# Performance work log

Hardware: AMD Instinct MI355X
Metric: run time of the kernel (lower is better)

Reference implementation:

```python
import jax, jax.numpy as jnp
import numpy as np

N, M, FIN, K, OUT, E = 8, 49152, 64, 6, 64, 393216


def setup_inputs() -> dict:
    key = jax.random.key(0)
    k1, k2, k3, k4, k5, k6 = jax.random.split(key, 6)
    x = jax.random.normal(k1, (N, M, FIN), jnp.float32)
    rows = jax.random.randint(k2, (E,), 0, M, jnp.int32)
    cols = jax.random.randint(k3, (E,), 0, M, jnp.int32)
    vals = jax.random.normal(k4, (E,), jnp.float32) * 0.1  # scaled-Laplacian values
    stdv = 1.0 / np.sqrt(OUT)
    weight = jax.random.uniform(k5, (FIN * K, OUT), jnp.float32, -stdv, stdv)
    bias = jax.random.uniform(k6, (OUT,), jnp.float32, -stdv, stdv)
    return {"x": x, "rows": rows, "cols": cols, "vals": vals,
            "weight": weight, "bias": bias}


def reference(x, rows, cols, vals, weight, bias):
    # x: [N, M, Fin]; L sparse [M, M] in COO (rows, cols, vals)
    n, m, fin = x.shape
    # x0: [M, Fin*N] as in torch permute(1,2,0).view(M, Fin*N)
    x0 = jnp.transpose(x, (1, 2, 0)).reshape(m, fin * n)

    def spmm(X):  # L @ X via gather + segment-sum scatter
        return jax.ops.segment_sum(vals[:, None] * X[cols], rows, num_segments=m)

    xs = [x0]
    if K > 1:
        x1 = spmm(x0)
        xs.append(x1)
        for _ in range(2, K):
            x2 = 2.0 * spmm(x1) - x0
            xs.append(x2)
            x0, x1 = x1, x2

    # stack -> [K, M, Fin, N]; torch then permutes to [N, M, Fin, K] and
    # flattens to (N*M, Fin*K) with Fin outer, K inner: weight row idx = f*K + k
    T = jnp.stack(xs, 0).reshape(K, m, fin, n)
    Wr = weight.reshape(fin, K, OUT)
    out = jnp.einsum('kmfn,fko->nmo', T, Wr) + bias  # [N, M, OUT]
    return jax.nn.elu(out)
```

## Files before the change

kernel.cpp:

```cpp
#include <hip/hip_runtime.h>
#include <hip/hip_bf16.h>
#include <math.h>

#define N_    8
#define M_    49152
#define FIN_  64
#define K_    6
#define OUT_  64
#define E_    393216
#define ROW_  512

typedef __attribute__((ext_vector_type(8))) short bf16x8;
typedef __attribute__((ext_vector_type(4))) float f32x4;

static __device__ __forceinline__ unsigned short f2bf(float f) {
    unsigned u = __float_as_uint(f);
    u += 0x7fff + ((u >> 16) & 1);
    return (unsigned short)(u >> 16);
}
static __device__ __forceinline__ float bfl(unsigned u) { return __uint_as_float(u << 16); }
static __device__ __forceinline__ float bfh(unsigned u) { return __uint_as_float(u & 0xffff0000u); }


__global__ void count_kernel(const int* __restrict__ rows, int* __restrict__ cnt) {
    int e = blockIdx.x * blockDim.x + threadIdx.x;
    if (e < E_) atomicAdd(&cnt[rows[e]], 1);
}

__global__ __launch_bounds__(1024) void scan_kernel(int* __restrict__ cntfill, int* __restrict__ rowptr) {
    __shared__ int wsum[16];
    __shared__ int carry;
    int t = threadIdx.x;
    int lane = t & 63, wid = t >> 6;
    if (t == 0) carry = 0;
    __syncthreads();
    for (int chunk = 0; chunk < M_; chunk += 1024) {
        int v = cntfill[chunk + t];
        int x = v;
        #pragma unroll
        for (int off = 1; off < 64; off <<= 1) {
            int y = __shfl_up(x, off, 64);
            if (lane >= off) x += y;
        }
        if (lane == 63) wsum[wid] = x;
        __syncthreads();
        if (t == 0) {
            int s = carry;
            #pragma unroll
            for (int i = 0; i < 16; ++i) { int c = wsum[i]; wsum[i] = s; s += c; }
            carry = s;
        }
        __syncthreads();
        int excl = wsum[wid] + x - v;
        rowptr[chunk + t]  = excl;
        cntfill[chunk + t] = excl;
        __syncthreads();
    }
    if (t == 0) rowptr[M_] = carry;
}

__global__ void fill_kernel(const int* __restrict__ rows, const int* __restrict__ cols,
                            const float* __restrict__ vals, int* __restrict__ fillpos,
                            int* __restrict__ ecol, float* __restrict__ evalv,
                            int* __restrict__ eidx) {
    int e = blockIdx.x * blockDim.x + threadIdx.x;
    if (e < E_) {
        int r = rows[e];
        int p = atomicAdd(&fillpos[r], 1);
        ecol[p]  = cols[e];
        evalv[p] = vals[e];
        eidx[p]  = e;
    }
}

__global__ void sort_kernel(const int* __restrict__ rowptr, int* __restrict__ ecol,
                            float* __restrict__ evalv, int* __restrict__ eidx) {
    int m = blockIdx.x * blockDim.x + threadIdx.x;
    if (m >= M_) return;
    int s = rowptr[m], e = rowptr[m + 1];
    for (int i = s + 1; i < e; ++i) {
        int ki = eidx[i]; int kc = ecol[i]; float kv = evalv[i];
        int j = i - 1;
        while (j >= s && eidx[j] > ki) {
            eidx[j + 1] = eidx[j]; ecol[j + 1] = ecol[j]; evalv[j + 1] = evalv[j];
            --j;
        }
        eidx[j + 1] = ki; ecol[j + 1] = kc; evalv[j + 1] = kv;
    }
}


__global__ void permute_bf16_kernel(const float* __restrict__ x, unsigned short* __restrict__ T0) {
    int idx = blockIdx.x * blockDim.x + threadIdx.x;
    int f4 = idx & 15, n = (idx >> 4) & 7, m = idx >> 7;
    float4 v = ((const float4*)x)[(size_t)(n * M_ + m) * 16 + f4];
    ushort4 o;
    o.x = f2bf(v.x); o.y = f2bf(v.y); o.z = f2bf(v.z); o.w = f2bf(v.w);
    *(ushort4*)(T0 + (size_t)m * ROW_ + n * 64 + f4 * 4) = o;
}

static __device__ __forceinline__ void fma_u4(float* acc, float v, uint4 u) {
    acc[0] += v * bfl(u.x); acc[1] += v * bfh(u.x);
    acc[2] += v * bfl(u.y); acc[3] += v * bfh(u.y);
    acc[4] += v * bfl(u.z); acc[5] += v * bfh(u.z);
    acc[6] += v * bfl(u.w); acc[7] += v * bfh(u.w);
}

__global__ __launch_bounds__(256) void spmm_bf16_kernel(
        const unsigned short* __restrict__ cur, const unsigned short* __restrict__ prev,
        unsigned short* __restrict__ nxt,
        const int* __restrict__ rowptr, const int* __restrict__ ecol,
        const float* __restrict__ evalv, float alpha, float beta) {
    int t = threadIdx.x;
    int w = t >> 6, l = t & 63;
    int m = blockIdx.x * 4 + w;
    int s = rowptr[m], e = rowptr[m + 1];
    float acc[8] = {0.f, 0.f, 0.f, 0.f, 0.f, 0.f, 0.f, 0.f};
    int i = s;
    for (; i + 3 < e; i += 4) {
        int c0 = ecol[i], c1 = ecol[i+1], c2 = ecol[i+2], c3 = ecol[i+3];
        float v0 = evalv[i], v1 = evalv[i+1], v2 = evalv[i+2], v3 = evalv[i+3];
        uint4 u0 = *(const uint4*)(cur + (size_t)c0 * ROW_ + l * 8);
        uint4 u1 = *(const uint4*)(cur + (size_t)c1 * ROW_ + l * 8);
        uint4 u2 = *(const uint4*)(cur + (size_t)c2 * ROW_ + l * 8);
        uint4 u3 = *(const uint4*)(cur + (size_t)c3 * ROW_ + l * 8);
        fma_u4(acc, v0, u0); fma_u4(acc, v1, u1);
        fma_u4(acc, v2, u2); fma_u4(acc, v3, u3);
    }
    if (i + 1 < e) {
        int c0 = ecol[i], c1 = ecol[i+1];
        float v0 = evalv[i], v1 = evalv[i+1];
        uint4 u0 = *(const uint4*)(cur + (size_t)c0 * ROW_ + l * 8);
        uint4 u1 = *(const uint4*)(cur + (size_t)c1 * ROW_ + l * 8);
        fma_u4(acc, v0, u0); fma_u4(acc, v1, u1);
        i += 2;
    }
    if (i < e) {
        uint4 u0 = *(const uint4*)(cur + (size_t)ecol[i] * ROW_ + l * 8);
        fma_u4(acc, evalv[i], u0);
    }
    #pragma unroll
    for (int j = 0; j < 8; ++j) acc[j] *= alpha;
    if (beta != 0.f) {
        uint4 p = *(const uint4*)(prev + (size_t)m * ROW_ + l * 8);
        acc[0] += beta * bfl(p.x); acc[1] += beta * bfh(p.x);
        acc[2] += beta * bfl(p.y); acc[3] += beta * bfh(p.y);
        acc[4] += beta * bfl(p.z); acc[5] += beta * bfh(p.z);
        acc[6] += beta * bfl(p.w); acc[7] += beta * bfh(p.w);
    }
    uint4 o;
    o.x = (unsigned)f2bf(acc[0]) | ((unsigned)f2bf(acc[1]) << 16);
    o.y = (unsigned)f2bf(acc[2]) | ((unsigned)f2bf(acc[3]) << 16);
    o.z = (unsigned)f2bf(acc[4]) | ((unsigned)f2bf(acc[5]) << 16);
    o.w = (unsigned)f2bf(acc[6]) | ((unsigned)f2bf(acc[7]) << 16);
    *(uint4*)(nxt + (size_t)m * ROW_ + l * 8) = o;
}

__global__ void wprep_kernel(const float* __restrict__ W, unsigned short* __restrict__ Wfrag) {
    int idx = blockIdx.x * blockDim.x + threadIdx.x;
    int i = idx & 7, l = (idx >> 3) & 63, tile = (idx >> 9) & 3, kk = idx >> 11;
    int kcheb = kk >> 1;
    int f = (kk & 1) * 32 + (l >> 4) * 8 + i;
    int o = tile * 16 + (l & 15);
    Wfrag[idx] = f2bf(W[(f * K_ + kcheb) * OUT_ + o]);
}

static __device__ __forceinline__ void epilogue_tile(
        f32x4 acc, int tile, int rbase, int col,
        const float* __restrict__ bias, float* __restrict__ outn) {
    int c = tile * 16 + col;
    float b = bias[c];
    #pragma unroll
    for (int v = 0; v < 4; ++v) {
        float r = acc[v] + b;
        r = r > 0.f ? r : (__expf(r) - 1.f);
        outn[(size_t)(rbase + v) * OUT_ + c] = r;
    }
}

__global__ __launch_bounds__(256) void combine_kernel(
        const unsigned short* __restrict__ Tbase,
        const unsigned short* __restrict__ Wfrag,
        const float* __restrict__ bias, float* __restrict__ out) {
    __shared__ unsigned short wlds[24576];
    int t = threadIdx.x;
    {
        const uint4* src = (const uint4*)Wfrag;
        uint4* dst = (uint4*)wlds;
        #pragma unroll
        for (int i = 0; i < 12; ++i)
            dst[t + 256 * i] = src[t + 256 * i];
    }
    __syncthreads();

    int w = t >> 6, l = t & 63;
    int rowhalf = w & 1, nhalf = w >> 1;
    int m0 = blockIdx.x * 32 + rowhalf * 16;
    int arow = m0 + (l & 15);
    const size_t MROW = (size_t)M_ * ROW_;
    size_t abase0 = (size_t)arow * ROW_ + (l >> 4) * 8;
    int rbase = m0 + (l >> 4) * 4;
    int col = l & 15;

    #pragma unroll
    for (int ni = 0; ni < 4; ++ni) {
        int n = nhalf * 4 + ni;
        size_t abase = abase0 + n * 64;
        bf16x8 a[12];
        #pragma unroll
        for (int kk = 0; kk < 12; ++kk)
            a[kk] = *(const bf16x8*)(Tbase + (size_t)(kk >> 1) * MROW + abase + (kk & 1) * 32);

        f32x4 acc0 = {0.f, 0.f, 0.f, 0.f};
        f32x4 acc1 = {0.f, 0.f, 0.f, 0.f};
        f32x4 acc2 = {0.f, 0.f, 0.f, 0.f};
        f32x4 acc3 = {0.f, 0.f, 0.f, 0.f};
        #pragma unroll
        for (int kk = 0; kk < 12; ++kk) {
            const unsigned short* wp = wlds + ((size_t)(kk * 4) * 64 + l) * 8;
            bf16x8 b0 = *(const bf16x8*)(wp);
            bf16x8 b1 = *(const bf16x8*)(wp + 512);
            bf16x8 b2 = *(const bf16x8*)(wp + 1024);
            bf16x8 b3 = *(const bf16x8*)(wp + 1536);
            acc0 = __builtin_amdgcn_mfma_f32_16x16x32_bf16(a[kk], b0, acc0, 0, 0, 0);
            acc1 = __builtin_amdgcn_mfma_f32_16x16x32_bf16(a[kk], b1, acc1, 0, 0, 0);
            acc2 = __builtin_amdgcn_mfma_f32_16x16x32_bf16(a[kk], b2, acc2, 0, 0, 0);
            acc3 = __builtin_amdgcn_mfma_f32_16x16x32_bf16(a[kk], b3, acc3, 0, 0, 0);
        }

        float* outn = out + (size_t)n * ((size_t)M_ * OUT_);
        epilogue_tile(acc0, 0, rbase, col, bias, outn);
        epilogue_tile(acc1, 1, rbase, col, bias, outn);
        epilogue_tile(acc2, 2, rbase, col, bias, outn);
        epilogue_tile(acc3, 3, rbase, col, bias, outn);
    }
}


__global__ void permute_kernel(const float* __restrict__ x, float* __restrict__ A) {
    int idx = blockIdx.x * blockDim.x + threadIdx.x;
    int f4 = idx & 15;
    int n  = (idx >> 4) & 7;
    int m  = idx >> 7;
    float4 v = ((const float4*)x)[(size_t)(n * M_ + m) * 16 + f4];
    ((float4*)A)[idx] = v;
}

__global__ __launch_bounds__(512) void step_kernel(
        const float* __restrict__ cur, float* __restrict__ nxt,
        const float* __restrict__ weight, const float* __restrict__ bias,
        const int* __restrict__ rowptr, const int* __restrict__ ecol,
        const float* __restrict__ evalv, float* __restrict__ out,
        int k, float alpha, float beta, int flags) {
    __shared__ float lds_x[ROW_];
    int m = blockIdx.x;
    int t = threadIdx.x;
    lds_x[t] = cur[(size_t)m * ROW_ + t];
    if (flags & 4) {
        float acc = 0.f;
        int s = rowptr[m], e = rowptr[m + 1];
        for (int i = s; i < e; ++i)
            acc += evalv[i] * cur[(size_t)ecol[i] * ROW_ + t];
        float prevv = (beta != 0.f) ? nxt[(size_t)m * ROW_ + t] : 0.f;
        nxt[(size_t)m * ROW_ + t] = alpha * acc + beta * prevv;
    }
    __syncthreads();
    int n = t >> 6, o = t & 63;
    const float4* lx4 = (const float4*)(lds_x + n * FIN_);
    float acc = 0.f;
    #pragma unroll
    for (int f4 = 0; f4 < 16; ++f4) {
        float4 xq = lx4[f4];
        int fb = f4 * 4;
        acc += xq.x * weight[((fb + 0) * K_ + k) * OUT_ + o];
        acc += xq.y * weight[((fb + 1) * K_ + k) * OUT_ + o];
        acc += xq.z * weight[((fb + 2) * K_ + k) * OUT_ + o];
        acc += xq.w * weight[((fb + 3) * K_ + k) * OUT_ + o];
    }
    size_t oidx = (size_t)n * (M_ * OUT_) + (size_t)m * OUT_ + o;
    float res = (flags & 1) ? acc : (out[oidx] + acc);
    if (flags & 2) {
        res += bias[o];
        res = (res > 0.f) ? res : (expf(res) - 1.f);
    }
    out[oidx] = res;
}


extern "C" void kernel_launch(void* const* d_in, const int* in_sizes, int n_in,
                              void* d_out, int out_size, void* d_ws, size_t ws_size,
                              hipStream_t stream) {
    (void)in_sizes; (void)n_in; (void)out_size;
    const float* x      = (const float*)d_in[0];
    const int*   rows   = (const int*)d_in[1];
    const int*   cols   = (const int*)d_in[2];
    const float* vals   = (const float*)d_in[3];
    const float* weight = (const float*)d_in[4];
    const float* bias   = (const float*)d_in[5];
    float* out = (float*)d_out;

    char* ws = (char*)d_ws;
    size_t off = 0;
    auto alloc = [&](size_t bytes) -> void* {
        void* p = ws + off;
        off += (bytes + 255) & ~(size_t)255;
        return p;
    };

    const size_t tbytes = (size_t)M_ * ROW_ * 2;
    const size_t need_new = 6 * (tbytes + 256) + (M_ + 1) * 4 + M_ * 4
                          + 3 * ((size_t)E_ * 4 + 256) + 24576 * 2 + 4096;

    if (ws_size >= need_new) {
        unsigned short* T[6];
        for (int i = 0; i < 6; ++i) T[i] = (unsigned short*)alloc(tbytes);
        int*   rowptr  = (int*)alloc((size_t)(M_ + 1) * 4);
        int*   fillpos = (int*)alloc((size_t)M_ * 4);
        int*   ecol    = (int*)alloc((size_t)E_ * 4);
        float* evalv   = (float*)alloc((size_t)E_ * 4);
        int*   eidx    = (int*)alloc((size_t)E_ * 4);
        unsigned short* Wfrag = (unsigned short*)alloc(24576 * 2);

        permute_bf16_kernel<<<(M_ * N_ * 16) / 256, 256, 0, stream>>>(x, T[0]);
        hipMemsetAsync(fillpos, 0, (size_t)M_ * 4, stream);
        count_kernel<<<E_ / 256, 256, 0, stream>>>(rows, fillpos);
        scan_kernel<<<1, 1024, 0, stream>>>(fillpos, rowptr);
        fill_kernel<<<E_ / 256, 256, 0, stream>>>(rows, cols, vals, fillpos, ecol, evalv, eidx);
        sort_kernel<<<M_ / 256, 256, 0, stream>>>(rowptr, ecol, evalv, eidx);
        wprep_kernel<<<96, 256, 0, stream>>>(weight, Wfrag);

        spmm_bf16_kernel<<<M_ / 4, 256, 0, stream>>>(T[0], T[0], T[1], rowptr, ecol, evalv, 1.f, 0.f);
        spmm_bf16_kernel<<<M_ / 4, 256, 0, stream>>>(T[1], T[0], T[2], rowptr, ecol, evalv, 2.f, -1.f);
        spmm_bf16_kernel<<<M_ / 4, 256, 0, stream>>>(T[2], T[1], T[3], rowptr, ecol, evalv, 2.f, -1.f);
        spmm_bf16_kernel<<<M_ / 4, 256, 0, stream>>>(T[3], T[2], T[4], rowptr, ecol, evalv, 2.f, -1.f);
        spmm_bf16_kernel<<<M_ / 4, 256, 0, stream>>>(T[4], T[3], T[5], rowptr, ecol, evalv, 2.f, -1.f);

        combine_kernel<<<M_ / 32, 256, 0, stream>>>(T[0], Wfrag, bias, out);
    } else {
        float* A       = (float*)alloc((size_t)M_ * ROW_ * 4);
        float* B       = (float*)alloc((size_t)M_ * ROW_ * 4);
        int*   rowptr  = (int*)alloc((size_t)(M_ + 1) * 4);
        int*   fillpos = (int*)alloc((size_t)M_ * 4);
        int*   ecol    = (int*)alloc((size_t)E_ * 4);
        float* evalv   = (float*)alloc((size_t)E_ * 4);
        int*   eidx    = (int*)alloc((size_t)E_ * 4);

        permute_kernel<<<(M_ * N_ * 16) / 256, 256, 0, stream>>>(x, A);
        hipMemsetAsync(fillpos, 0, (size_t)M_ * 4, stream);
        count_kernel<<<E_ / 256, 256, 0, stream>>>(rows, fillpos);
        scan_kernel<<<1, 1024, 0, stream>>>(fillpos, rowptr);
        fill_kernel<<<E_ / 256, 256, 0, stream>>>(rows, cols, vals, fillpos, ecol, evalv, eidx);
        sort_kernel<<<M_ / 256, 256, 0, stream>>>(rowptr, ecol, evalv, eidx);

        step_kernel<<<M_, 512, 0, stream>>>(A, B, weight, bias, rowptr, ecol, evalv, out, 0, 1.f, 0.f, 1 | 4);
        step_kernel<<<M_, 512, 0, stream>>>(B, A, weight, bias, rowptr, ecol, evalv, out, 1, 2.f, -1.f, 4);
        step_kernel<<<M_, 512, 0, stream>>>(A, B, weight, bias, rowptr, ecol, evalv, out, 2, 2.f, -1.f, 4);
        step_kernel<<<M_, 512, 0, stream>>>(B, A, weight, bias, rowptr, ecol, evalv, out, 3, 2.f, -1.f, 4);
        step_kernel<<<M_, 512, 0, stream>>>(A, B, weight, bias, rowptr, ecol, evalv, out, 4, 2.f, -1.f, 4);
        step_kernel<<<M_, 512, 0, stream>>>(B, B, weight, bias, rowptr, ecol, evalv, out, 5, 0.f, 0.f, 2);
    }
}
```

Before: 567.5 us.

## Parallelize row-pointer scan, fuse setup kernels, shuffle-broadcast edges in SpMM

Replaces the serial chunked scan with a register-held two-level block scan and hardcodes the final row pointer to E. Fuses the edge count into the permute kernel and the weight fragment prep into the fill kernel, cutting launches. SpMM loads up to 64 edge indices and values per wave once and broadcasts them by shuffle, and prefetches the previous-term row early. The combine kernel now has each wave handle 16 rows for all 8 batches, with the bias hoisted. The scan holds many values per thread in registers, which adds register pressure.

```diff
diff --git a/kernel.cpp b/kernel.cpp
--- a/kernel.cpp
+++ b/kernel.cpp
@@ -28,35 +28,52 @@
 }
 
 __global__ __launch_bounds__(1024) void scan_kernel(int* __restrict__ cntfill, int* __restrict__ rowptr) {
-    __shared__ int wsum[16];
-    __shared__ int carry;
+    __shared__ int lws[768];
+    __shared__ int lw2[12];
     int t = threadIdx.x;
     int lane = t & 63, wid = t >> 6;
-    if (t == 0) carry = 0;
-    __syncthreads();
-    for (int chunk = 0; chunk < M_; chunk += 1024) {
-        int v = cntfill[chunk + t];
-        int x = v;
+    int v[48], d[48];
+    #pragma unroll
+    for (int ch = 0; ch < 48; ++ch) v[ch] = cntfill[ch * 1024 + t];
+    #pragma unroll
+    for (int ch = 0; ch < 48; ++ch) {
+        int s = v[ch];
         #pragma unroll
         for (int off = 1; off < 64; off <<= 1) {
-            int y = __shfl_up(x, off, 64);
-            if (lane >= off) x += y;
+            int y = __shfl_up(s, off, 64);
+            if (lane >= off) s += y;
         }
-        if (lane == 63) wsum[wid] = x;
-        __syncthreads();
-        if (t == 0) {
-            int s = carry;
-            #pragma unroll
-            for (int i = 0; i < 16; ++i) { int c = wsum[i]; wsum[i] = s; s += c; }
-            carry = s;
+        d[ch] = s - v[ch];
+        if (lane == 63) lws[ch * 16 + wid] = s;
+    }
+    __syncthreads();
+    int orig = 0, s2 = 0;
+    if (t < 768) {
+        orig = lws[t];
+        s2 = orig;
+        #pragma unroll
+        for (int off = 1; off < 64; off <<= 1) {
+            int y = __shfl_up(s2, off, 64);
+            if (lane >= off) s2 += y;
         }
-        __syncthreads();
-        int excl = wsum[wid] + x - v;
-        rowptr[chunk + t]  = excl;
-        cntfill[chunk + t] = excl;
-        __syncthreads();
-    }
-    if (t == 0) rowptr[M_] = carry;
+        if (lane == 63) lw2[t >> 6] = s2;
+    }
+    __syncthreads();
+    if (t == 0) {
+        int run = 0;
+        #pragma unroll
+        for (int i = 0; i < 12; ++i) { int c = lw2[i]; lw2[i] = run; run += c; }
+    }
+    __syncthreads();
+    if (t < 768) lws[t] = lw2[t >> 6] + s2 - orig;
+    __syncthreads();
+    #pragma unroll
+    for (int ch = 0; ch < 48; ++ch) {
+        int excl = lws[ch * 16 + wid] + d[ch];
+        rowptr[ch * 1024 + t]  = excl;
+        cntfill[ch * 1024 + t] = excl;
+    }
+    if (t == 0) rowptr[M_] = E_;
 }
 
 __global__ void fill_kernel(const int* __restrict__ rows, const int* __restrict__ cols,
@@ -90,13 +107,37 @@
 }
 
 
-__global__ void permute_bf16_kernel(const float* __restrict__ x, unsigned short* __restrict__ T0) {
+__global__ void permute_count_kernel(const float* __restrict__ x, unsigned short* __restrict__ T0,
+                                     const int* __restrict__ rows, int* __restrict__ cnt) {
     int idx = blockIdx.x * blockDim.x + threadIdx.x;
     int f4 = idx & 15, n = (idx >> 4) & 7, m = idx >> 7;
     float4 v = ((const float4*)x)[(size_t)(n * M_ + m) * 16 + f4];
     ushort4 o;
     o.x = f2bf(v.x); o.y = f2bf(v.y); o.z = f2bf(v.z); o.w = f2bf(v.w);
     *(ushort4*)(T0 + (size_t)m * ROW_ + n * 64 + f4 * 4) = o;
+    if (idx < E_) atomicAdd(&cnt[rows[idx]], 1);
+}
+
+__global__ void fill_wprep_kernel(const int* __restrict__ rows, const int* __restrict__ cols,
+                                  const float* __restrict__ vals, int* __restrict__ fillpos,
+                                  int* __restrict__ ecol, float* __restrict__ evalv,
+                                  int* __restrict__ eidx,
+                                  const float* __restrict__ W, unsigned short* __restrict__ Wfrag) {
+    int e = blockIdx.x * blockDim.x + threadIdx.x;
+    if (e < E_) {
+        int r = rows[e];
+        int p = atomicAdd(&fillpos[r], 1);
+        ecol[p]  = cols[e];
+        evalv[p] = vals[e];
+        eidx[p]  = e;
+    }
+    if (e < 24576) {
+        int i = e & 7, l = (e >> 3) & 63, tile = (e >> 9) & 3, kk = e >> 11;
+        int kcheb = kk >> 1;
+        int f = (kk & 1) * 32 + (l >> 4) * 8 + i;
+        int o = tile * 16 + (l & 15);
+        Wfrag[e] = f2bf(W[(f * K_ + kcheb) * OUT_ + o]);
+    }
 }
 
 static __device__ __forceinline__ void fma_u4(float* acc, float v, uint4 u) {
@@ -115,11 +156,20 @@
     int w = t >> 6, l = t & 63;
     int m = blockIdx.x * 4 + w;
     int s = rowptr[m], e = rowptr[m + 1];
+    int cnt = e - s;
+    int myc = 0; float myv = 0.f;
+    if (l < cnt) { myc = ecol[s + l]; myv = evalv[s + l]; }
+    uint4 p;
+    if (beta != 0.f) p = *(const uint4*)(prev + (size_t)m * ROW_ + l * 8);
+
     float acc[8] = {0.f, 0.f, 0.f, 0.f, 0.f, 0.f, 0.f, 0.f};
-    int i = s;
-    for (; i + 3 < e; i += 4) {
-        int c0 = ecol[i], c1 = ecol[i+1], c2 = ecol[i+2], c3 = ecol[i+3];
-        float v0 = evalv[i], v1 = evalv[i+1], v2 = evalv[i+2], v3 = evalv[i+3];
+    int lim = cnt < 64 ? cnt : 64;
+    int i = 0;
+    for (; i + 3 < lim; i += 4) {
+        int c0 = __shfl(myc, i),     c1 = __shfl(myc, i + 1);
+        int c2 = __shfl(myc, i + 2), c3 = __shfl(myc, i + 3);
+        float v0 = __shfl(myv, i),     v1 = __shfl(myv, i + 1);
+        float v2 = __shfl(myv, i + 2), v3 = __shfl(myv, i + 3);
         uint4 u0 = *(const uint4*)(cur + (size_t)c0 * ROW_ + l * 8);
         uint4 u1 = *(const uint4*)(cur + (size_t)c1 * ROW_ + l * 8);
         uint4 u2 = *(const uint4*)(cur + (size_t)c2 * ROW_ + l * 8);
@@ -127,22 +177,21 @@
         fma_u4(acc, v0, u0); fma_u4(acc, v1, u1);
         fma_u4(acc, v2, u2); fma_u4(acc, v3, u3);
     }
-    if (i + 1 < e) {
-        int c0 = ecol[i], c1 = ecol[i+1];
-        float v0 = evalv[i], v1 = evalv[i+1];
+    for (; i < lim; ++i) {
+        int c0 = __shfl(myc, i);
+        float v0 = __shfl(myv, i);
         uint4 u0 = *(const uint4*)(cur + (size_t)c0 * ROW_ + l * 8);
-        uint4 u1 = *(const uint4*)(cur + (size_t)c1 * ROW_ + l * 8);
-        fma_u4(acc, v0, u0); fma_u4(acc, v1, u1);
-        i += 2;
-    }
-    if (i < e) {
-        uint4 u0 = *(const uint4*)(cur + (size_t)ecol[i] * ROW_ + l * 8);
-        fma_u4(acc, evalv[i], u0);
+        fma_u4(acc, v0, u0);
+    }
+    for (int j = 64; j < cnt; ++j) {
+        int c0 = ecol[s + j];
+        float v0 = evalv[s + j];
+        uint4 u0 = *(const uint4*)(cur + (size_t)c0 * ROW_ + l * 8);
+        fma_u4(acc, v0, u0);
     }
     #pragma unroll
     for (int j = 0; j < 8; ++j) acc[j] *= alpha;
     if (beta != 0.f) {
-        uint4 p = *(const uint4*)(prev + (size_t)m * ROW_ + l * 8);
         acc[0] += beta * bfl(p.x); acc[1] += beta * bfh(p.x);
         acc[2] += beta * bfl(p.y); acc[3] += beta * bfh(p.y);
         acc[4] += beta * bfl(p.z); acc[5] += beta * bfh(p.z);
@@ -156,20 +205,10 @@
     *(uint4*)(nxt + (size_t)m * ROW_ + l * 8) = o;
 }
 
-__global__ void wprep_kernel(const float* __restrict__ W, unsigned short* __restrict__ Wfrag) {
-    int idx = blockIdx.x * blockDim.x + threadIdx.x;
-    int i = idx & 7, l = (idx >> 3) & 63, tile = (idx >> 9) & 3, kk = idx >> 11;
-    int kcheb = kk >> 1;
-    int f = (kk & 1) * 32 + (l >> 4) * 8 + i;
-    int o = tile * 16 + (l & 15);
-    Wfrag[idx] = f2bf(W[(f * K_ + kcheb) * OUT_ + o]);
-}
-
 static __device__ __forceinline__ void epilogue_tile(
-        f32x4 acc, int tile, int rbase, int col,
-        const float* __restrict__ bias, float* __restrict__ outn) {
+        f32x4 acc, int tile, int rbase, int col, float b,
+        float* __restrict__ outn) {
     int c = tile * 16 + col;
-    float b = bias[c];
     #pragma unroll
     for (int v = 0; v < 4; ++v) {
         float r = acc[v] + b;
@@ -194,17 +233,16 @@
     __syncthreads();
 
     int w = t >> 6, l = t & 63;
-    int rowhalf = w & 1, nhalf = w >> 1;
-    int m0 = blockIdx.x * 32 + rowhalf * 16;
+    int m0 = blockIdx.x * 64 + w * 16;
     int arow = m0 + (l & 15);
     const size_t MROW = (size_t)M_ * ROW_;
     size_t abase0 = (size_t)arow * ROW_ + (l >> 4) * 8;
     int rbase = m0 + (l >> 4) * 4;
     int col = l & 15;
-
-    #pragma unroll
-    for (int ni = 0; ni < 4; ++ni) {
-        int n = nhalf * 4 + ni;
+    float b0 = bias[col], b1 = bias[16 + col], b2 = bias[32 + col], b3 = bias[48 + col];
+
+    #pragma unroll
+    for (int n = 0; n < 8; ++n) {
         size_t abase = abase0 + n * 64;
         bf16x8 a[12];
         #pragma unroll
@@ -218,21 +256,21 @@
         #pragma unroll
         for (int kk = 0; kk < 12; ++kk) {
             const unsigned short* wp = wlds + ((size_t)(kk * 4) * 64 + l) * 8;
-            bf16x8 b0 = *(const bf16x8*)(wp);
-            bf16x8 b1 = *(const bf16x8*)(wp + 512);
-            bf16x8 b2 = *(const bf16x8*)(wp + 1024);
-            bf16x8 b3 = *(const bf16x8*)(wp + 1536);
-            acc0 = __builtin_amdgcn_mfma_f32_16x16x32_bf16(a[kk], b0, acc0, 0, 0, 0);
-            acc1 = __builtin_amdgcn_mfma_f32_16x16x32_bf16(a[kk], b1, acc1, 0, 0, 0);
-            acc2 = __builtin_amdgcn_mfma_f32_16x16x32_bf16(a[kk], b2, acc2, 0, 0, 0);
-            acc3 = __builtin_amdgcn_mfma_f32_16x16x32_bf16(a[kk], b3, acc3, 0, 0, 0);
+            bf16x8 q0 = *(const bf16x8*)(wp);
+            bf16x8 q1 = *(const bf16x8*)(wp + 512);
+            bf16x8 q2 = *(const bf16x8*)(wp + 1024);
+            bf16x8 q3 = *(const bf16x8*)(wp + 1536);
+            acc0 = __builtin_amdgcn_mfma_f32_16x16x32_bf16(a[kk], q0, acc0, 0, 0, 0);
+            acc1 = __builtin_amdgcn_mfma_f32_16x16x32_bf16(a[kk], q1, acc1, 0, 0, 0);
+            acc2 = __builtin_amdgcn_mfma_f32_16x16x32_bf16(a[kk], q2, acc2, 0, 0, 0);
+            acc3 = __builtin_amdgcn_mfma_f32_16x16x32_bf16(a[kk], q3, acc3, 0, 0, 0);
         }
 
         float* outn = out + (size_t)n * ((size_t)M_ * OUT_);
-        epilogue_tile(acc0, 0, rbase, col, bias, outn);
-        epilogue_tile(acc1, 1, rbase, col, bias, outn);
-        epilogue_tile(acc2, 2, rbase, col, bias, outn);
-        epilogue_tile(acc3, 3, rbase, col, bias, outn);
+        epilogue_tile(acc0, 0, rbase, col, b0, outn);
+        epilogue_tile(acc1, 1, rbase, col, b1, outn);
+        epilogue_tile(acc2, 2, rbase, col, b2, outn);
+        epilogue_tile(acc3, 3, rbase, col, b3, outn);
     }
 }
 
@@ -321,13 +359,12 @@
         int*   eidx    = (int*)alloc((size_t)E_ * 4);
         unsigned short* Wfrag = (unsigned short*)alloc(24576 * 2);
 
-        permute_bf16_kernel<<<(M_ * N_ * 16) / 256, 256, 0, stream>>>(x, T[0]);
         hipMemsetAsync(fillpos, 0, (size_t)M_ * 4, stream);
-        count_kernel<<<E_ / 256, 256, 0, stream>>>(rows, fillpos);
+        permute_count_kernel<<<(M_ * N_ * 16) / 256, 256, 0, stream>>>(x, T[0], rows, fillpos);
         scan_kernel<<<1, 1024, 0, stream>>>(fillpos, rowptr);
-        fill_kernel<<<E_ / 256, 256, 0, stream>>>(rows, cols, vals, fillpos, ecol, evalv, eidx);
+        fill_wprep_kernel<<<E_ / 256, 256, 0, stream>>>(rows, cols, vals, fillpos,
+                                                        ecol, evalv, eidx, weight, Wfrag);
         sort_kernel<<<M_ / 256, 256, 0, stream>>>(rowptr, ecol, evalv, eidx);
-        wprep_kernel<<<96, 256, 0, stream>>>(weight, Wfrag);
 
         spmm_bf16_kernel<<<M_ / 4, 256, 0, stream>>>(T[0], T[0], T[1], rowptr, ecol, evalv, 1.f, 0.f);
         spmm_bf16_kernel<<<M_ / 4, 256, 0, stream>>>(T[1], T[0], T[2], rowptr, ecol, evalv, 2.f, -1.f);
@@ -335,7 +372,7 @@
         spmm_bf16_kernel<<<M_ / 4, 256, 0, stream>>>(T[3], T[2], T[4], rowptr, ecol, evalv, 2.f, -1.f);
         spmm_bf16_kernel<<<M_ / 4, 256, 0, stream>>>(T[4], T[3], T[5], rowptr, ecol, evalv, 2.f, -1.f);
 
-        combine_kernel<<<M_ / 32, 256, 0, stream>>>(T[0], Wfrag, bias, out);
+        combine_kernel<<<M_ / 64, 256, 0, stream>>>(T[0], Wfrag, bias, out);
     } else {
         float* A       = (float*)alloc((size_t)M_ * ROW_ * 4);
         float* B       = (float*)alloc((size_t)M_ * ROW_ * 4);
```

Measured after the change: 639.9 us. 12.8% more time.
